# Kernel tuning notes

Hardware: AMD Instinct MI355X
Metric: run time of the kernel (lower is better)

## Reference

```python
import jax, jax.numpy as jnp
import numpy as np

EPS = 1e-4  # BatchNorm eps from module


def setup_inputs() -> dict:
    key = jax.random.key(0)
    ks = jax.random.split(key, 7)
    N, C, H, W = 4, 256, 64, 64
    D = C  # reduction=1
    x = jax.random.normal(ks[0], (N, C, H, W), dtype=jnp.float32)
    # 1x1 conv weights, msra-style scaled init
    s = 1.0 / np.sqrt(C)
    Wq = jax.random.normal(ks[1], (D, C), dtype=jnp.float32) * s
    Wk = jax.random.normal(ks[2], (D, C), dtype=jnp.float32) * s
    Wv = jax.random.normal(ks[3], (D, C), dtype=jnp.float32) * s
    Wo = jax.random.normal(ks[4], (C, D), dtype=jnp.float32) * s
    gamma = jnp.ones((C,), dtype=jnp.float32)
    beta = jnp.zeros((C,), dtype=jnp.float32)
    return {"x": x, "Wq": Wq, "Wk": Wk, "Wv": Wv, "Wo": Wo, "gamma": gamma, "beta": beta}


def reference(x, Wq, Wk, Wv, Wo, gamma, beta):
    N, C, H, W = x.shape
    D = Wq.shape[0]
    scale = 1.0 / jnp.sqrt(jnp.float32(D))
    xf = x.reshape(N, C, H * W)                      # (N, C, L)
    # 1x1 convs == per-position linear projections
    q = jnp.einsum('dc,ncl->nld', Wq, xf)            # (N, L, D)
    k = jnp.einsum('dc,ncl->nld', Wk, xf)            # (N, L, D)
    v = jnp.einsum('dc,ncl->nld', Wv, xf)            # (N, L, D)
    scores = jnp.einsum('nld,nmd->nlm', q, k) * scale  # (N, L, L)
    attn = jax.nn.softmax(scores, axis=2)
    out = jnp.einsum('nlm,nmd->nld', attn, v)        # (N, L, D)
    out = jnp.einsum('od,nld->nol', Wo, out).reshape(N, C, H, W)
    # BatchNorm2d (training-mode batch statistics, biased variance)
    mean = jnp.mean(out, axis=(0, 2, 3), keepdims=True)
    var = jnp.var(out, axis=(0, 2, 3), keepdims=True)
    out = (out - mean) * jax.lax.rsqrt(var + EPS)
    out = out * gamma[None, :, None, None] + beta[None, :, None, None]
    return x + out
```

## Files before the change

### kernel.cpp

```cpp
#include <hip/hip_runtime.h>
#include <cstdint>
#include <cstddef>

#define NB 4
#define CH 256
#define LL 4096

typedef unsigned short u16;
typedef unsigned int u32;
typedef unsigned char u8;
typedef __attribute__((ext_vector_type(8))) short bf16x8;
typedef __attribute__((ext_vector_type(4))) float f32x4;

#define GPTR(p) ((const __attribute__((address_space(1))) u32*)(p))
#define LPTR(p) ((__attribute__((address_space(3))) u32*)(p))

__device__ __forceinline__ float blo(u32 x) { return __uint_as_float(x << 16); }
__device__ __forceinline__ float bhi(u32 x) { return __uint_as_float(x & 0xffff0000u); }
__device__ __forceinline__ float b2f(u16 h) { return __uint_as_float(((u32)h) << 16); }
__device__ __forceinline__ u16 f2b(float f) {
    u32 u = __float_as_uint(f);
    u32 r = (u + 0x7fffu + ((u >> 16) & 1u)) >> 16;
    return (u16)r;
}
__device__ __forceinline__ u32 pack2(float a, float b) {
    return (u32)f2b(a) | ((u32)f2b(b) << 16);
}

__global__ __launch_bounds__(256) void prep_kernel(
    const float* __restrict__ x, const float* __restrict__ Wq,
    const float* __restrict__ Wk, const float* __restrict__ Wv,
    const float* __restrict__ Wo, u16* __restrict__ Wb,
    float* __restrict__ stats, u16* __restrict__ xT) {
    const int id = blockIdx.x;
    const int tid = threadIdx.x;
    __shared__ u16 t[64][72];
    if (id < 1024) {
        const int n = id >> 8;
        const int c0 = ((id >> 6) & 3) * 64, l0 = (id & 63) * 64;
        const float* xs = x + (size_t)n * CH * LL;
        const int lq = (tid & 15) * 4, cc = tid >> 4;
#pragma unroll
        for (int p = 0; p < 4; ++p) {
            int c = cc + p * 16;
            float4 v = *(const float4*)&xs[(size_t)(c0 + c) * LL + l0 + lq];
            t[lq + 0][c] = f2b(v.x);
            t[lq + 1][c] = f2b(v.y);
            t[lq + 2][c] = f2b(v.z);
            t[lq + 3][c] = f2b(v.w);
        }
        __syncthreads();
        u16* xo = xT + (size_t)n * LL * CH;
        const int l = tid >> 2, c8 = (tid & 3) * 16;
#pragma unroll
        for (int h = 0; h < 2; ++h) {
            uint4 vv = *(uint4*)&t[l][c8 + h * 8];
            *(uint4*)&xo[(size_t)(l0 + l) * CH + c0 + c8 + h * 8] = vv;
        }
    } else {
        const int j = id - 1024;
        const int i = (j & 63) * 256 + tid;
        const int m = j >> 6;
        if (m == 0 && (j & 63) < 2) stats[i] = 0.0f;
        const float* src = (m == 0) ? Wq : (m == 1) ? Wk : (m == 2) ? Wv : Wo;
        float4 v = ((const float4*)src)[i];
        uint2 o;
        o.x = pack2(v.x, v.y);
        o.y = pack2(v.z, v.w);
        ((uint2*)(Wb + m * 65536))[i] = o;
    }
}

__global__ __launch_bounds__(256, 2) void proj_kernel(
    const u16* __restrict__ xT, const u16* __restrict__ Wb,
    u16* __restrict__ q, u16* __restrict__ k, u16* __restrict__ vT) {
    const int id = blockIdx.x;
    const int tid = threadIdx.x;
    const int w = tid >> 6, lane = tid & 63;
    const int lhi = lane >> 4, llo = lane & 15;

    __shared__ __align__(16) u16 Bs[128 * 256];

    if (id < 1024) {
        const int n = id >> 8;
        const int yy = (id >> 6) & 3;
        const int dhalf = yy & 1, mat = yy >> 1;
        const int l0 = (id & 63) * 64;
        const int d0 = dhalf * 128;

        const u16* xn = xT + (size_t)n * LL * CH;
        const u16* Wm = Wb + mat * 65536 + (size_t)d0 * CH;

#pragma unroll
        for (int i = 0; i < 16; ++i) {
            int s = i * 256 + tid;
            int r = s >> 5, c = s & 31;
            __builtin_amdgcn_global_load_lds(GPTR(Wm + r * CH + (c ^ (r & 31)) * 8),
                                             LPTR((char*)Bs + i * 4096 + w * 1024),
                                             16, 0, 0);
        }

        bf16x8 af[8];
        const u16* abase = xn + (size_t)(l0 + w * 16 + llo) * CH + lhi * 8;
#pragma unroll
        for (int ks = 0; ks < 8; ++ks) af[ks] = *(const bf16x8*)(abase + ks * 32);

        f32x4 acc[8];
#pragma unroll
        for (int t = 0; t < 8; ++t) acc[t] = (f32x4){0.f, 0.f, 0.f, 0.f};

        __syncthreads();

#pragma unroll
        for (int ks = 0; ks < 8; ++ks) {
#pragma unroll
            for (int ct = 0; ct < 8; ++ct) {
                const int rr = ct * 16 + llo;
                bf16x8 bf = *(const bf16x8*)(Bs + rr * CH +
                                             ((ks * 4 + lhi) ^ (rr & 31)) * 8);
                acc[ct] = __builtin_amdgcn_mfma_f32_16x16x32_bf16(af[ks], bf, acc[ct], 0, 0, 0);
            }
        }

        u16* o = (mat ? k : q) + (size_t)n * LL * CH;
#pragma unroll
        for (int r = 0; r < 4; ++r) {
            int lr = l0 + w * 16 + lhi * 4 + r;
#pragma unroll
            for (int ct = 0; ct < 8; ++ct)
                o[(size_t)lr * CH + d0 + ct * 16 + llo] = f2b(acc[ct][r]);
        }
    } else {
        const int j = id - 1024;
        const int n = j >> 7;
        const int d0 = ((j >> 5) & 3) * 64;
        const int l0 = (j & 31) * 128;

        const u16* xn = xT + (size_t)n * LL * CH + (size_t)l0 * CH;
        const u16* Wm = Wb + 2 * 65536;

#pragma unroll
        for (int i = 0; i < 16; ++i) {
            int s = i * 256 + tid;
            int r = s >> 5, c = s & 31;
            __builtin_amdgcn_global_load_lds(GPTR(xn + r * CH + (c ^ (r & 31)) * 8),
                                             LPTR((char*)Bs + i * 4096 + w * 1024),
                                             16, 0, 0);
        }

        bf16x8 af[8];
        const u16* abase = Wm + (size_t)(d0 + w * 16 + llo) * CH + lhi * 8;
#pragma unroll
        for (int ks = 0; ks < 8; ++ks) af[ks] = *(const bf16x8*)(abase + ks * 32);

        f32x4 acc[8];
#pragma unroll
        for (int t = 0; t < 8; ++t) acc[t] = (f32x4){0.f, 0.f, 0.f, 0.f};

        __syncthreads();

#pragma unroll
        for (int ks = 0; ks < 8; ++ks) {
#pragma unroll
            for (int ct = 0; ct < 8; ++ct) {
                const int rr = ct * 16 + llo;
                bf16x8 bf = *(const bf16x8*)(Bs + rr * CH +
                                             ((ks * 4 + lhi) ^ (rr & 31)) * 8);
                acc[ct] = __builtin_amdgcn_mfma_f32_16x16x32_bf16(af[ks], bf, acc[ct], 0, 0, 0);
            }
        }

        u16* o = vT + (size_t)n * CH * LL;
#pragma unroll
        for (int r = 0; r < 4; ++r) {
            int dr = d0 + w * 16 + lhi * 4 + r;
#pragma unroll
            for (int ct = 0; ct < 8; ++ct)
                o[(size_t)dr * LL + l0 + ct * 16 + llo] = f2b(acc[ct][r]);
        }
    }
}

__global__ __launch_bounds__(256, 2) void fattn_kernel(
    const u16* __restrict__ q, const u16* __restrict__ k,
    const u16* __restrict__ vT, u16* __restrict__ Op, float* __restrict__ l_s,
    int iters) {
    const int n = blockIdx.y;
    const int s_id = blockIdx.z;
    const int l0 = blockIdx.x * 128;
    const int m_base = s_id * iters * 32;
    const int tid = threadIdx.x;
    const int w = tid >> 6;
    const int lane = tid & 63;
    const int lhi = lane >> 4, llo = lane & 15;

    __shared__ __align__(16) char smem[65536];

    bf16x8 qf[2][8];
    {
        const u16* base = q + (size_t)(n * LL + l0 + w * 32 + llo) * CH + lhi * 8;
#pragma unroll
        for (int t = 0; t < 2; ++t)
#pragma unroll
            for (int ks = 0; ks < 8; ++ks)
                qf[t][ks] = *(const bf16x8*)(base + t * 16 * CH + ks * 32);
    }

    const u16* kg = k + (size_t)n * LL * CH;
    const u16* vg = vT + (size_t)n * CH * LL;

    int okK[4], okV[4];
#pragma unroll
    for (int i = 0; i < 4; ++i) {
        int s = i * 256 + tid;
        int rK = s >> 5;
        int cK = (s & 31) ^ rK;
        okK[i] = rK * CH + cK * 8;
        int dV = s >> 2;
        int cV = (s & 3) ^ ((dV & 3) ^ ((dV >> 2) & 3));
        okV[i] = dV * LL + cV * 8;
    }

    f32x4 oacc[2][16];
#pragma unroll
    for (int t = 0; t < 2; ++t)
#pragma unroll
        for (int ct = 0; ct < 16; ++ct) oacc[t][ct] = (f32x4){0.f, 0.f, 0.f, 0.f};
    float lrun[2] = {0.f, 0.f};

    const float C1 = 0.09016844005556021f;
    const int posV = (lhi ^ ((llo & 3) ^ (llo >> 2))) * 8;
    const int idxA = (llo + 32 * (lhi & 1)) * 4;
    const int idxB = idxA + 64;
    const bool selLo = (lhi < 2);

    {
        const u16* kg2 = kg + (size_t)m_base * CH;
        const u16* vg2 = vg + m_base;
#pragma unroll
        for (int i = 0; i < 4; ++i) {
            __builtin_amdgcn_global_load_lds(GPTR(kg2 + okK[i]),
                                             LPTR(smem + i * 4096 + w * 1024), 16, 0, 0);
            __builtin_amdgcn_global_load_lds(GPTR(vg2 + okV[i]),
                                             LPTR(smem + 32768 + i * 4096 + w * 1024),
                                             16, 0, 0);
        }
    }

    for (int it = 0; it < iters; ++it) {
        __syncthreads();
        if (it + 1 < iters) {
            const int m1 = m_base + (it + 1) * 32;
            const u16* kg2 = kg + (size_t)m1 * CH;
            const u16* vg2 = vg + m1;
            char* Kb = smem + ((it + 1) & 1) * 16384;
            char* Vb = smem + 32768 + ((it + 1) & 1) * 16384;
#pragma unroll
            for (int i = 0; i < 4; ++i) {
                __builtin_amdgcn_global_load_lds(GPTR(kg2 + okK[i]),
                                                 LPTR(Kb + i * 4096 + w * 1024), 16, 0, 0);
                __builtin_amdgcn_global_load_lds(GPTR(vg2 + okV[i]),
                                                 LPTR(Vb + i * 4096 + w * 1024), 16, 0, 0);
            }
        }
        const u16* Kl = (const u16*)(smem + (it & 1) * 16384);
        const u16* Vl = (const u16*)(smem + 32768 + (it & 1) * 16384);

        f32x4 s00 = (f32x4){0.f, 0.f, 0.f, 0.f};
        f32x4 s01 = (f32x4){0.f, 0.f, 0.f, 0.f};
        f32x4 s10 = (f32x4){0.f, 0.f, 0.f, 0.f};
        f32x4 s11 = (f32x4){0.f, 0.f, 0.f, 0.f};
        __builtin_amdgcn_s_setprio(1);
#pragma unroll
        for (int ks = 0; ks < 8; ++ks) {
            const int cq = ks * 4 + lhi;
            bf16x8 b0 = *(const bf16x8*)(Kl + llo * 256 + (cq ^ llo) * 8);
            bf16x8 b1 = *(const bf16x8*)(Kl + (llo + 16) * 256 + (cq ^ (llo + 16)) * 8);
            s00 = __builtin_amdgcn_mfma_f32_16x16x32_bf16(b0, qf[0][ks], s00, 0, 0, 0);
            s10 = __builtin_amdgcn_mfma_f32_16x16x32_bf16(b0, qf[1][ks], s10, 0, 0, 0);
            s01 = __builtin_amdgcn_mfma_f32_16x16x32_bf16(b1, qf[0][ks], s01, 0, 0, 0);
            s11 = __builtin_amdgcn_mfma_f32_16x16x32_bf16(b1, qf[1][ks], s11, 0, 0, 0);
        }
        __builtin_amdgcn_s_setprio(0);

        bf16x8 pa[2];
#pragma unroll
        for (int qt = 0; qt < 2; ++qt) {
            f32x4 sa = qt ? s10 : s00;
            f32x4 sb = qt ? s11 : s01;
            float pA0 = __builtin_amdgcn_exp2f(sa[0] * C1);
            float pA1 = __builtin_amdgcn_exp2f(sa[1] * C1);
            float pA2 = __builtin_amdgcn_exp2f(sa[2] * C1);
            float pA3 = __builtin_amdgcn_exp2f(sa[3] * C1);
            float pB0 = __builtin_amdgcn_exp2f(sb[0] * C1);
            float pB1 = __builtin_amdgcn_exp2f(sb[1] * C1);
            float pB2 = __builtin_amdgcn_exp2f(sb[2] * C1);
            float pB3 = __builtin_amdgcn_exp2f(sb[3] * C1);
            lrun[qt] += ((pA0 + pA1) + (pA2 + pA3)) + ((pB0 + pB1) + (pB2 + pB3));
            u32 w0, w1, w2, w3;
            asm("v_cvt_pk_bf16_f32 %0, %1, %2" : "=v"(w0) : "v"(pA0), "v"(pA1));
            asm("v_cvt_pk_bf16_f32 %0, %1, %2" : "=v"(w1) : "v"(pA2), "v"(pA3));
            asm("v_cvt_pk_bf16_f32 %0, %1, %2" : "=v"(w2) : "v"(pB0), "v"(pB1));
            asm("v_cvt_pk_bf16_f32 %0, %1, %2" : "=v"(w3) : "v"(pB2), "v"(pB3));
            int t0 = __builtin_amdgcn_ds_bpermute(idxA, (int)w0);
            int t2 = __builtin_amdgcn_ds_bpermute(idxA, (int)w2);
            int u0 = __builtin_amdgcn_ds_bpermute(idxA, (int)w1);
            int u2 = __builtin_amdgcn_ds_bpermute(idxA, (int)w3);
            int v0 = __builtin_amdgcn_ds_bpermute(idxB, (int)w0);
            int v2 = __builtin_amdgcn_ds_bpermute(idxB, (int)w2);
            int x0 = __builtin_amdgcn_ds_bpermute(idxB, (int)w1);
            int x2 = __builtin_amdgcn_ds_bpermute(idxB, (int)w3);
            union { u32 u[4]; bf16x8 v; } pk;
            pk.u[0] = selLo ? (u32)t0 : (u32)t2;
            pk.u[1] = selLo ? (u32)u0 : (u32)u2;
            pk.u[2] = selLo ? (u32)v0 : (u32)v2;
            pk.u[3] = selLo ? (u32)x0 : (u32)x2;
            pa[qt] = pk.v;
        }

        __builtin_amdgcn_s_setprio(1);
#pragma unroll
        for (int ct = 0; ct < 16; ++ct) {
            bf16x8 vf = *(const bf16x8*)(Vl + (ct * 16 + llo) * 32 + posV);
            oacc[0][ct] = __builtin_amdgcn_mfma_f32_16x16x32_bf16(pa[0], vf, oacc[0][ct], 0, 0, 0);
            oacc[1][ct] = __builtin_amdgcn_mfma_f32_16x16x32_bf16(pa[1], vf, oacc[1][ct], 0, 0, 0);
        }
        __builtin_amdgcn_s_setprio(0);
    }

    u16* ap = Op + (size_t)((s_id * NB + n) * (size_t)LL + l0 + w * 32) * CH;
    float* lp = l_s + (size_t)s_id * NB * LL + (size_t)n * LL + l0 + w * 32;
#pragma unroll
    for (int t = 0; t < 2; ++t) {
        float ls = lrun[t];
        ls += __shfl_xor(ls, 16);
        ls += __shfl_xor(ls, 32);
        if (lhi == 0) lp[t * 16 + llo] = ls;
#pragma unroll
        for (int r = 0; r < 4; ++r) {
            int lrow = t * 16 + lhi * 4 + r;
#pragma unroll
            for (int ct = 0; ct < 16; ++ct) {
                ap[(size_t)lrow * CH + ct * 16 + llo] = f2b(oacc[t][ct][r]);
            }
        }
    }
}

__global__ __launch_bounds__(256) void merge_kernel(
    const u16* __restrict__ Op, const float* __restrict__ l_s,
    u16* __restrict__ att, int S) {
    const size_t t8 = (size_t)blockIdx.x * 256 + threadIdx.x;
    const size_t flat = t8 * 8;
    const size_t row = flat >> 8;
    float lsum = 0.0f;
    for (int s = 0; s < S; ++s) lsum += l_s[(size_t)s * NB * LL + row];
    const float inv = 1.0f / lsum;
    float acc[8];
#pragma unroll
    for (int j = 0; j < 8; ++j) acc[j] = 0.0f;
    for (int s = 0; s < S; ++s) {
        uint4 raw = *(const uint4*)(Op + (size_t)s * NB * LL * CH + flat);
        acc[0] += blo(raw.x); acc[1] += bhi(raw.x);
        acc[2] += blo(raw.y); acc[3] += bhi(raw.y);
        acc[4] += blo(raw.z); acc[5] += bhi(raw.z);
        acc[6] += blo(raw.w); acc[7] += bhi(raw.w);
    }
    uint4 o;
    o.x = pack2(acc[0] * inv, acc[1] * inv);
    o.y = pack2(acc[2] * inv, acc[3] * inv);
    o.z = pack2(acc[4] * inv, acc[5] * inv);
    o.w = pack2(acc[6] * inv, acc[7] * inv);
    *(uint4*)(att + flat) = o;
}

__global__ __launch_bounds__(256, 2) void outm_kernel(
    const u16* __restrict__ Wb, const u16* __restrict__ att,
    u16* __restrict__ y, float* __restrict__ stats) {
    const int n = blockIdx.z;
    const int o0 = blockIdx.y * 64;
    const int l0 = blockIdx.x * 128;
    const int tid = threadIdx.x;
    const int w = tid >> 6, lane = tid & 63;
    const int lhi = lane >> 4, llo = lane & 15;

    __shared__ __align__(16) u16 Bs[128 * 256];

    const u16* an = att + (size_t)n * LL * CH + (size_t)l0 * CH;
    const u16* Wm = Wb + 3 * 65536;

#pragma unroll
    for (int i = 0; i < 16; ++i) {
        int s = i * 256 + tid;
        int r = s >> 5, c = s & 31;
        __builtin_amdgcn_global_load_lds(GPTR(an + r * CH + (c ^ (r & 31)) * 8),
                                         LPTR((char*)Bs + i * 4096 + w * 1024),
                                         16, 0, 0);
    }

    bf16x8 af[8];
    const u16* abase = Wm + (size_t)(o0 + w * 16 + llo) * CH + lhi * 8;
#pragma unroll
    for (int ks = 0; ks < 8; ++ks) af[ks] = *(const bf16x8*)(abase + ks * 32);

    f32x4 acc[8];
#pragma unroll
    for (int t = 0; t < 8; ++t) acc[t] = (f32x4){0.f, 0.f, 0.f, 0.f};

    __syncthreads();

#pragma unroll
    for (int ks = 0; ks < 8; ++ks) {
#pragma unroll
        for (int ct = 0; ct < 8; ++ct) {
            const int rr = ct * 16 + llo;
            bf16x8 bf = *(const bf16x8*)(Bs + rr * CH +
                                         ((ks * 4 + lhi) ^ (rr & 31)) * 8);
            acc[ct] = __builtin_amdgcn_mfma_f32_16x16x32_bf16(af[ks], bf, acc[ct], 0, 0, 0);
        }
    }

    u16* yn = y + (size_t)n * CH * LL;
#pragma unroll
    for (int r = 0; r < 4; ++r) {
        const int orow = o0 + w * 16 + lhi * 4 + r;
        float ts = 0.0f, tq = 0.0f;
#pragma unroll
        for (int ct = 0; ct < 8; ++ct) {
            float vv = acc[ct][r];
            yn[(size_t)orow * LL + l0 + ct * 16 + llo] = f2b(vv);
            ts += vv;
            tq += vv * vv;
        }
        ts += __shfl_xor(ts, 1); tq += __shfl_xor(tq, 1);
        ts += __shfl_xor(ts, 2); tq += __shfl_xor(tq, 2);
        ts += __shfl_xor(ts, 4); tq += __shfl_xor(tq, 4);
        ts += __shfl_xor(ts, 8); tq += __shfl_xor(tq, 8);
        if (llo == 0) {
            atomicAdd(&stats[orow], ts);
            atomicAdd(&stats[256 + orow], tq);
        }
    }
}

__global__ __launch_bounds__(256) void bn_kernel(
    const float* __restrict__ x, const u16* __restrict__ y,
    const float* __restrict__ stats, const float* __restrict__ gamma,
    const float* __restrict__ beta, float* __restrict__ out) {
    const int idx = blockIdx.x * 256 + threadIdx.x;
    const int base = idx * 4;
    const int c = (base >> 12) & 255;
    const float cnt = 1.0f / 16384.0f;
    float mean = stats[c] * cnt;
    float var = stats[256 + c] * cnt - mean * mean;
    float rstd = rsqrtf(var + 1e-4f);
    float g = gamma[c] * rstd;
    float b = beta[c];
    uint2 yv = ((const uint2*)y)[idx];
    float4 xv = ((const float4*)x)[idx];
    float4 o;
    o.x = xv.x + (blo(yv.x) - mean) * g + b;
    o.y = xv.y + (bhi(yv.x) - mean) * g + b;
    o.z = xv.z + (blo(yv.y) - mean) * g + b;
    o.w = xv.w + (bhi(yv.y) - mean) * g + b;
    ((float4*)out)[idx] = o;
}

extern "C" void kernel_launch(void* const* d_in, const int* in_sizes, int n_in,
                              void* d_out, int out_size, void* d_ws, size_t ws_size,
                              hipStream_t stream) {
    const float* x = (const float*)d_in[0];
    const float* Wq = (const float*)d_in[1];
    const float* Wk = (const float*)d_in[2];
    const float* Wv = (const float*)d_in[3];
    const float* Wo = (const float*)d_in[4];
    const float* gamma = (const float*)d_in[5];
    const float* beta = (const float*)d_in[6];
    float* out = (float*)d_out;

    const size_t elems = (size_t)NB * LL * CH;

    int S = 1;
    for (int cand = 4; cand >= 2; cand >>= 1) {
        size_t need = elems * 2 * (size_t)(3 + cand) +
                      (size_t)cand * NB * LL * 4 + 524288 + 8192;
        if (ws_size >= need) { S = cand; break; }
    }
    const int iters = 128 / S;

    char* wsb = (char*)d_ws;
    u16* q = (u16*)wsb;
    u16* k = q + elems;
    u16* vT = k + elems;
    u16* Op = vT + elems;
    u16* xT = Op;
    float* l_s = (float*)(Op + (size_t)S * elems);
    u16* Wb = (u16*)(l_s + (size_t)S * NB * LL);
    float* stats = (float*)(Wb + 4 * 65536);
    u16* att = q;
    u16* y = k;

    prep_kernel<<<1280, 256, 0, stream>>>(x, Wq, Wk, Wv, Wo, Wb, stats, xT);
    proj_kernel<<<1536, 256, 0, stream>>>(xT, Wb, q, k, vT);
    fattn_kernel<<<dim3(LL / 128, NB, S), 256, 0, stream>>>(q, k, vT, Op, l_s, iters);
    merge_kernel<<<(int)(elems / 8 / 256), 256, 0, stream>>>(Op, l_s, att, S);
    outm_kernel<<<dim3(LL / 128, CH / 64, NB), 256, 0, stream>>>(Wb, att, y, stats);
    bn_kernel<<<(NB * CH * LL / 4) / 256, 256, 0, stream>>>(x, y, stats, gamma, beta, out);
}
```

Measured before the change: 203.7 us.

## Switch attention kernel to 32x32x16 MFMA tiles with permlane32 swap

Rewrites the flash-attention inner loop to use 32x32x16 bf16 MFMA instructions instead of 16x16x32, for both QK^T and PV. Each wave now computes a 32x32 score tile with one accumulator. The P operand is re-laid out with v_permlane32_swap instead of eight ds_bpermute calls plus selects. This is meant to cut instruction count, LDS permute traffic and K/V fragment reads per FLOP. The larger MFMA has longer latency and a different accumulator layout, which risks correctness and register pressure.

```diff
diff --git a/kernel.cpp b/kernel.cpp
--- a/kernel.cpp
+++ b/kernel.cpp
@@ -11,6 +11,7 @@
 typedef unsigned char u8;
 typedef __attribute__((ext_vector_type(8))) short bf16x8;
 typedef __attribute__((ext_vector_type(4))) float f32x4;
+typedef __attribute__((ext_vector_type(16))) float f32x16;
 
 #define GPTR(p) ((const __attribute__((address_space(1))) u32*)(p))
 #define LPTR(p) ((__attribute__((address_space(3))) u32*)(p))
@@ -192,18 +193,16 @@
     const int tid = threadIdx.x;
     const int w = tid >> 6;
     const int lane = tid & 63;
-    const int lhi = lane >> 4, llo = lane & 15;
+    const int l31 = lane & 31;
+    const int h = lane >> 5;
 
     __shared__ __align__(16) char smem[65536];
 
-    bf16x8 qf[2][8];
+    bf16x8 qf[16];
     {
-        const u16* base = q + (size_t)(n * LL + l0 + w * 32 + llo) * CH + lhi * 8;
-#pragma unroll
-        for (int t = 0; t < 2; ++t)
-#pragma unroll
-            for (int ks = 0; ks < 8; ++ks)
-                qf[t][ks] = *(const bf16x8*)(base + t * 16 * CH + ks * 32);
+        const u16* base = q + (size_t)(n * LL + l0 + w * 32 + l31) * CH + h * 8;
+#pragma unroll
+        for (int s = 0; s < 16; ++s) qf[s] = *(const bf16x8*)(base + s * 16);
     }
 
     const u16* kg = k + (size_t)n * LL * CH;
@@ -221,18 +220,16 @@
         okV[i] = dV * LL + cV * 8;
     }
 
-    f32x4 oacc[2][16];
-#pragma unroll
-    for (int t = 0; t < 2; ++t)
-#pragma unroll
-        for (int ct = 0; ct < 16; ++ct) oacc[t][ct] = (f32x4){0.f, 0.f, 0.f, 0.f};
-    float lrun[2] = {0.f, 0.f};
+    f32x16 oacc[8];
+#pragma unroll
+    for (int t = 0; t < 8; ++t)
+        oacc[t] = (f32x16){0.f, 0.f, 0.f, 0.f, 0.f, 0.f, 0.f, 0.f,
+                           0.f, 0.f, 0.f, 0.f, 0.f, 0.f, 0.f, 0.f};
+    float lrun = 0.f;
 
     const float C1 = 0.09016844005556021f;
-    const int posV = (lhi ^ ((llo & 3) ^ (llo >> 2))) * 8;
-    const int idxA = (llo + 32 * (lhi & 1)) * 4;
-    const int idxB = idxA + 64;
-    const bool selLo = (lhi < 2);
+    const int kx = h ^ l31;
+    const int hg = h ^ ((lane & 3) ^ ((lane >> 2) & 3));
 
     {
         const u16* kg2 = kg + (size_t)m_base * CH;
@@ -266,83 +263,66 @@
         const u16* Kl = (const u16*)(smem + (it & 1) * 16384);
         const u16* Vl = (const u16*)(smem + 32768 + (it & 1) * 16384);
 
-        f32x4 s00 = (f32x4){0.f, 0.f, 0.f, 0.f};
-        f32x4 s01 = (f32x4){0.f, 0.f, 0.f, 0.f};
-        f32x4 s10 = (f32x4){0.f, 0.f, 0.f, 0.f};
-        f32x4 s11 = (f32x4){0.f, 0.f, 0.f, 0.f};
+        f32x16 sacc = (f32x16){0.f, 0.f, 0.f, 0.f, 0.f, 0.f, 0.f, 0.f,
+                               0.f, 0.f, 0.f, 0.f, 0.f, 0.f, 0.f, 0.f};
         __builtin_amdgcn_s_setprio(1);
 #pragma unroll
-        for (int ks = 0; ks < 8; ++ks) {
-            const int cq = ks * 4 + lhi;
-            bf16x8 b0 = *(const bf16x8*)(Kl + llo * 256 + (cq ^ llo) * 8);
-            bf16x8 b1 = *(const bf16x8*)(Kl + (llo + 16) * 256 + (cq ^ (llo + 16)) * 8);
-            s00 = __builtin_amdgcn_mfma_f32_16x16x32_bf16(b0, qf[0][ks], s00, 0, 0, 0);
-            s10 = __builtin_amdgcn_mfma_f32_16x16x32_bf16(b0, qf[1][ks], s10, 0, 0, 0);
-            s01 = __builtin_amdgcn_mfma_f32_16x16x32_bf16(b1, qf[0][ks], s01, 0, 0, 0);
-            s11 = __builtin_amdgcn_mfma_f32_16x16x32_bf16(b1, qf[1][ks], s11, 0, 0, 0);
+        for (int s = 0; s < 16; ++s) {
+            bf16x8 af = *(const bf16x8*)(Kl + l31 * 256 + ((2 * s) ^ kx) * 8);
+            sacc = __builtin_amdgcn_mfma_f32_32x32x16_bf16(af, qf[s], sacc, 0, 0, 0);
         }
         __builtin_amdgcn_s_setprio(0);
 
+        u32 W[4][2];
+#pragma unroll
+        for (int g = 0; g < 4; ++g) {
+            float p0 = __builtin_amdgcn_exp2f(sacc[4 * g + 0] * C1);
+            float p1 = __builtin_amdgcn_exp2f(sacc[4 * g + 1] * C1);
+            float p2 = __builtin_amdgcn_exp2f(sacc[4 * g + 2] * C1);
+            float p3 = __builtin_amdgcn_exp2f(sacc[4 * g + 3] * C1);
+            lrun += (p0 + p1) + (p2 + p3);
+            asm("v_cvt_pk_bf16_f32 %0, %1, %2" : "=v"(W[g][0]) : "v"(p0), "v"(p1));
+            asm("v_cvt_pk_bf16_f32 %0, %1, %2" : "=v"(W[g][1]) : "v"(p2), "v"(p3));
+        }
+
         bf16x8 pa[2];
 #pragma unroll
-        for (int qt = 0; qt < 2; ++qt) {
-            f32x4 sa = qt ? s10 : s00;
-            f32x4 sb = qt ? s11 : s01;
-            float pA0 = __builtin_amdgcn_exp2f(sa[0] * C1);
-            float pA1 = __builtin_amdgcn_exp2f(sa[1] * C1);
-            float pA2 = __builtin_amdgcn_exp2f(sa[2] * C1);
-            float pA3 = __builtin_amdgcn_exp2f(sa[3] * C1);
-            float pB0 = __builtin_amdgcn_exp2f(sb[0] * C1);
-            float pB1 = __builtin_amdgcn_exp2f(sb[1] * C1);
-            float pB2 = __builtin_amdgcn_exp2f(sb[2] * C1);
-            float pB3 = __builtin_amdgcn_exp2f(sb[3] * C1);
-            lrun[qt] += ((pA0 + pA1) + (pA2 + pA3)) + ((pB0 + pB1) + (pB2 + pB3));
-            u32 w0, w1, w2, w3;
-            asm("v_cvt_pk_bf16_f32 %0, %1, %2" : "=v"(w0) : "v"(pA0), "v"(pA1));
-            asm("v_cvt_pk_bf16_f32 %0, %1, %2" : "=v"(w1) : "v"(pA2), "v"(pA3));
-            asm("v_cvt_pk_bf16_f32 %0, %1, %2" : "=v"(w2) : "v"(pB0), "v"(pB1));
-            asm("v_cvt_pk_bf16_f32 %0, %1, %2" : "=v"(w3) : "v"(pB2), "v"(pB3));
-            int t0 = __builtin_amdgcn_ds_bpermute(idxA, (int)w0);
-            int t2 = __builtin_amdgcn_ds_bpermute(idxA, (int)w2);
-            int u0 = __builtin_amdgcn_ds_bpermute(idxA, (int)w1);
-            int u2 = __builtin_amdgcn_ds_bpermute(idxA, (int)w3);
-            int v0 = __builtin_amdgcn_ds_bpermute(idxB, (int)w0);
-            int v2 = __builtin_amdgcn_ds_bpermute(idxB, (int)w2);
-            int x0 = __builtin_amdgcn_ds_bpermute(idxB, (int)w1);
-            int x2 = __builtin_amdgcn_ds_bpermute(idxB, (int)w3);
+        for (int sp = 0; sp < 2; ++sp) {
+            u32 a0 = W[2 * sp][0], b0 = W[2 * sp + 1][0];
+            asm("v_permlane32_swap_b32 %0, %1" : "+v"(a0), "+v"(b0));
+            u32 a1 = W[2 * sp][1], b1 = W[2 * sp + 1][1];
+            asm("v_permlane32_swap_b32 %0, %1" : "+v"(a1), "+v"(b1));
             union { u32 u[4]; bf16x8 v; } pk;
-            pk.u[0] = selLo ? (u32)t0 : (u32)t2;
-            pk.u[1] = selLo ? (u32)u0 : (u32)u2;
-            pk.u[2] = selLo ? (u32)v0 : (u32)v2;
-            pk.u[3] = selLo ? (u32)x0 : (u32)x2;
-            pa[qt] = pk.v;
+            pk.u[0] = a0;
+            pk.u[1] = a1;
+            pk.u[2] = b0;
+            pk.u[3] = b1;
+            pa[sp] = pk.v;
         }
 
         __builtin_amdgcn_s_setprio(1);
 #pragma unroll
-        for (int ct = 0; ct < 16; ++ct) {
-            bf16x8 vf = *(const bf16x8*)(Vl + (ct * 16 + llo) * 32 + posV);
-            oacc[0][ct] = __builtin_amdgcn_mfma_f32_16x16x32_bf16(pa[0], vf, oacc[0][ct], 0, 0, 0);
-            oacc[1][ct] = __builtin_amdgcn_mfma_f32_16x16x32_bf16(pa[1], vf, oacc[1][ct], 0, 0, 0);
+        for (int sp = 0; sp < 2; ++sp) {
+#pragma unroll
+            for (int dt = 0; dt < 8; ++dt) {
+                bf16x8 vf = *(const bf16x8*)(Vl + (dt * 32 + l31) * 32 +
+                                             ((2 * sp) ^ hg) * 8);
+                oacc[dt] = __builtin_amdgcn_mfma_f32_32x32x16_bf16(pa[sp], vf, oacc[dt], 0, 0, 0);
+            }
         }
         __builtin_amdgcn_s_setprio(0);
     }
 
     u16* ap = Op + (size_t)((s_id * NB + n) * (size_t)LL + l0 + w * 32) * CH;
     float* lp = l_s + (size_t)s_id * NB * LL + (size_t)n * LL + l0 + w * 32;
-#pragma unroll
-    for (int t = 0; t < 2; ++t) {
-        float ls = lrun[t];
-        ls += __shfl_xor(ls, 16);
-        ls += __shfl_xor(ls, 32);
-        if (lhi == 0) lp[t * 16 + llo] = ls;
-#pragma unroll
-        for (int r = 0; r < 4; ++r) {
-            int lrow = t * 16 + lhi * 4 + r;
-#pragma unroll
-            for (int ct = 0; ct < 16; ++ct) {
-                ap[(size_t)lrow * CH + ct * 16 + llo] = f2b(oacc[t][ct][r]);
-            }
+    lrun += __shfl_xor(lrun, 32);
+    if (h == 0) lp[l31] = lrun;
+#pragma unroll
+    for (int dt = 0; dt < 8; ++dt) {
+#pragma unroll
+        for (int r = 0; r < 16; ++r) {
+            int qrow = (r & 3) + 8 * (r >> 2) + 4 * h;
+            ap[(size_t)qrow * CH + dt * 32 + l31] = f2b(oacc[dt][r]);
         }
     }
 }
```

Measured after the change: 197.4 us. 3.1% less time.
